# Performance work log

Hardware: AMD Instinct MI355X
Metric: run time of the kernel (lower is better)

## Reference

```python
import jax, jax.numpy as jnp
import numpy as np

B, H, N, D = 4, 4, 2048, 64

def setup_inputs() -> dict:
    key = jax.random.key(0)
    kq, kk, kv, km = jax.random.split(key, 4)
    q = jax.random.normal(kq, (B, H, N, D), dtype=jnp.float32)
    k = jax.random.normal(kk, (B, H, N, D), dtype=jnp.float32)
    v = jax.random.normal(kv, (B, H, N, D), dtype=jnp.float32)
    mask = jax.random.randint(km, (B, N), 0, 2, dtype=jnp.int32)
    return {"q": q, "k": k, "v": v, "mask": mask}

def reference(q, k, v, mask):
    # scores: [B, H, Nq, Nk]
    scale = jnp.asarray(q.shape[-1] ** 0.5, q.dtype)
    scores = jnp.einsum('bhid,bhjd->bhij', q, k) / scale
    neg = jnp.finfo(scores.dtype).min
    m = mask[:, None, None, :]  # [B,1,1,Nk]
    scores = jnp.where(m == 0, neg, scores)
    attention = jax.nn.softmax(scores, axis=-1)
    output = jnp.einsum('bhij,bhjd->bhid', attention, v)
    return (output, attention)
```

## Files before the change

kernel.cpp:

```cpp
#include <hip/hip_runtime.h>

typedef __attribute__((ext_vector_type(8))) short short8;
typedef __attribute__((ext_vector_type(4))) float f32x4;

#define NHEADS 16
#define N_ 2048
#define D_ 64
#define ROWS 16
#define LDP 2056
#define NT 256
#define MT 512

__device__ __forceinline__ unsigned short f2b(float f) {
    unsigned u = __float_as_uint(f);
    return (unsigned short)((u + 0x7FFFu + ((u >> 16) & 1u)) >> 16);
}
__device__ __forceinline__ float b2f(unsigned short b) {
    return __uint_as_float(((unsigned)b) << 16);
}

__global__ __launch_bounds__(NT)
void cvt_bf16_kernel(const float4* __restrict__ src, ushort4* __restrict__ dst, int n4)
{
    int i = blockIdx.x * NT + threadIdx.x;
    if (i < n4) {
        float4 v = src[i];
        ushort4 o;
        o.x = f2b(v.x); o.y = f2b(v.y); o.z = f2b(v.z); o.w = f2b(v.w);
        dst[i] = o;
    }
}

__global__ __launch_bounds__(NT)
void vtrans_kernel(const float* __restrict__ v, unsigned short* __restrict__ vt)
{
    __shared__ float tile[64][65];
    const int head = blockIdx.x >> 5;
    const int k0   = (blockIdx.x & 31) * 64;
    const int tid  = threadIdx.x;

    {
        const int i = tid >> 2;
        const int c = tid & 3;
        const float4* v4 = (const float4*)(v + ((size_t)(head * N_ + k0 + i)) * D_);
        #pragma unroll
        for (int u = 0; u < 4; ++u) {
            const int c4 = c + 4 * u;
            float4 val = v4[c4];
            tile[i][c4 * 4 + 0] = val.x;
            tile[i][c4 * 4 + 1] = val.y;
            tile[i][c4 * 4 + 2] = val.z;
            tile[i][c4 * 4 + 3] = val.w;
        }
    }
    __syncthreads();
    {
        const int d  = tid >> 2;
        const int kk = (tid & 3) * 16;
        unsigned short* dst = vt + ((size_t)(head * D_ + d)) * N_ + k0 + kk;
        #pragma unroll
        for (int m4 = 0; m4 < 4; ++m4) {
            ushort4 ov;
            ov.x = f2b(tile[kk + m4 * 4 + 0][d]);
            ov.y = f2b(tile[kk + m4 * 4 + 1][d]);
            ov.z = f2b(tile[kk + m4 * 4 + 2][d]);
            ov.w = f2b(tile[kk + m4 * 4 + 3][d]);
            *(ushort4*)(dst + m4 * 4) = ov;
        }
    }
}

__global__ __launch_bounds__(MT, 4)
void lg_attn(const unsigned short* __restrict__ Qb,
             const unsigned short* __restrict__ Kb,
             const unsigned short* __restrict__ Vt,
             const int* __restrict__ mask,
             float* __restrict__ out,
             float* __restrict__ attn)
{
    __shared__ unsigned short P[ROWS * LDP];
    __shared__ float wred[128];

    const int tid  = threadIdx.x;
    const int w    = tid >> 6;
    const int lane = tid & 63;
    const int quad = lane >> 4;
    const int l16  = lane & 15;

    const int head = blockIdx.x >> 7;
    const int it   = blockIdx.x & 127;
    const int i0   = it * ROWS;
    const int bidx = head >> 2;

    const unsigned short* qrow = Qb + ((size_t)(head * N_ + i0 + l16)) * D_ + quad * 8;
    const short8 a0 = *(const short8*)qrow;
    const short8 a1 = *(const short8*)(qrow + 32);

    const unsigned short* kbase = Kb + (size_t)head * N_ * D_;
    const int* mrow = mask + bidx * N_;

    float s4[4] = {0.f, 0.f, 0.f, 0.f};
    #pragma unroll 4
    for (int t = 0; t < 16; ++t) {
        const int j0 = (w + 8 * t) * 16;
        const unsigned short* krow = kbase + (size_t)(j0 + l16) * D_ + quad * 8;
        short8 b0 = *(const short8*)krow;
        short8 b1 = *(const short8*)(krow + 32);
        f32x4 cc = {0.f, 0.f, 0.f, 0.f};
        cc = __builtin_amdgcn_mfma_f32_16x16x32_bf16(a0, b0, cc, 0, 0, 0);
        cc = __builtin_amdgcn_mfma_f32_16x16x32_bf16(a1, b1, cc, 0, 0, 0);
        const int mv = mrow[j0 + l16];
        #pragma unroll
        for (int r = 0; r < 4; ++r) {
            const float e = __expf(cc[r] * 0.125f);
            const float p = (mv == 0) ? 0.f : e;
            s4[r] += p;
            P[(quad * 4 + r) * LDP + j0 + l16] = f2b(p);
        }
    }

    #pragma unroll
    for (int r = 0; r < 4; ++r)
        #pragma unroll
        for (int off = 1; off < 16; off <<= 1)
            s4[r] += __shfl_xor(s4[r], off, 64);
    if (l16 == 0) {
        #pragma unroll
        for (int r = 0; r < 4; ++r) wred[w * 16 + quad * 4 + r] = s4[r];
    }
    __syncthreads();

    if (w >= 4) {
        const int tid2 = tid - 256;
        const size_t abase = (size_t)(head * N_ + i0) * N_;
        #pragma unroll 1
        for (int r = 0; r < ROWS; ++r) {
            float s = 0.f;
            #pragma unroll
            for (int ww = 0; ww < 8; ++ww) s += wred[ww * 16 + r];
            const float inv = 1.0f / s;
            f32x4* arow = (f32x4*)(attn + abase + (size_t)r * N_);
            #pragma unroll
            for (int u = 0; u < 2; ++u) {
                const int c4 = tid2 + u * 256;
                ushort4 tv = *(ushort4*)&P[r * LDP + c4 * 4];
                f32x4 f;
                f.x = b2f(tv.x) * inv;
                f.y = b2f(tv.y) * inv;
                f.z = b2f(tv.z) * inv;
                f.w = b2f(tv.w) * inv;
                __builtin_nontemporal_store(f, &arow[c4]);
            }
        }
    } else {
        const int n0 = w * 16;
        const unsigned short* vbase =
            Vt + ((size_t)(head * D_ + n0 + l16)) * N_ + quad * 8;
        f32x4 o = {0.f, 0.f, 0.f, 0.f};
        #pragma unroll 4
        for (int kc = 0; kc < 64; ++kc) {
            short8 ap = *(short8*)&P[l16 * LDP + kc * 32 + quad * 8];
            short8 bv = *(const short8*)(vbase + kc * 32);
            o = __builtin_amdgcn_mfma_f32_16x16x32_bf16(ap, bv, o, 0, 0, 0);
        }
        #pragma unroll
        for (int r = 0; r < 4; ++r) {
            const int row = quad * 4 + r;
            float s = 0.f;
            #pragma unroll
            for (int ww = 0; ww < 8; ++ww) s += wred[ww * 16 + row];
            out[((size_t)(head * N_ + i0 + row)) * D_ + n0 + l16] = o[r] / s;
        }
    }
}

extern "C" void kernel_launch(void* const* d_in, const int* in_sizes, int n_in,
                              void* d_out, int out_size, void* d_ws, size_t ws_size,
                              hipStream_t stream) {
    const float* q    = (const float*)d_in[0];
    const float* k    = (const float*)d_in[1];
    const float* v    = (const float*)d_in[2];
    const int*   mask = (const int*)d_in[3];

    float* out  = (float*)d_out;
    float* attn = out + (size_t)NHEADS * N_ * D_;

    const size_t elems = (size_t)NHEADS * N_ * D_;
    unsigned short* Qb = (unsigned short*)d_ws;
    unsigned short* Kb = Qb + elems;
    unsigned short* Vt = Kb + elems;

    const int n4 = (int)(elems / 4);
    const int cblocks = (n4 + NT - 1) / NT;
    cvt_bf16_kernel<<<cblocks, NT, 0, stream>>>((const float4*)q, (ushort4*)Qb, n4);
    cvt_bf16_kernel<<<cblocks, NT, 0, stream>>>((const float4*)k, (ushort4*)Kb, n4);
    vtrans_kernel<<<NHEADS * 32, NT, 0, stream>>>(v, Vt);

    lg_attn<<<NHEADS * 128, MT, 0, stream>>>(Qb, Kb, Vt, mask, out, attn);
}
```

Measured before the change: 382.4 us.

## Fuse Q conversion into attention kernel and merge K/V prep into one launch

The separate Q fp32-to-bf16 kernel is removed; each attention block now loads Q in fp32 and converts it to bf16 in registers. The K conversion and the V transpose are merged into one prep kernel, which cuts the launch count from four to two. The attention-write loop now reads eight bf16 values per thread with a single 16-byte LDS load and issues two stores. The cost is a slightly larger Q read per block (fp32 instead of bf16), and the prep kernel's K blocks still reserve the shared tile.

```diff
diff --git a/kernel.cpp b/kernel.cpp
--- a/kernel.cpp
+++ b/kernel.cpp
@@ -11,6 +11,9 @@
 #define NT 256
 #define MT 512
 
+#define KCVT_BLOCKS 2048
+#define VT_BLOCKS   512
+
 __device__ __forceinline__ unsigned short f2b(float f) {
     unsigned u = __float_as_uint(f);
     return (unsigned short)((u + 0x7FFFu + ((u >> 16) & 1u)) >> 16);
@@ -20,23 +23,21 @@
 }
 
 __global__ __launch_bounds__(NT)
-void cvt_bf16_kernel(const float4* __restrict__ src, ushort4* __restrict__ dst, int n4)
-{
-    int i = blockIdx.x * NT + threadIdx.x;
-    if (i < n4) {
-        float4 v = src[i];
-        ushort4 o;
-        o.x = f2b(v.x); o.y = f2b(v.y); o.z = f2b(v.z); o.w = f2b(v.w);
-        dst[i] = o;
-    }
-}
-
-__global__ __launch_bounds__(NT)
-void vtrans_kernel(const float* __restrict__ v, unsigned short* __restrict__ vt)
+void prep_kernel(const float4* __restrict__ k, const float* __restrict__ v,
+                 ushort4* __restrict__ Kb, unsigned short* __restrict__ vt)
 {
     __shared__ float tile[64][65];
-    const int head = blockIdx.x >> 5;
-    const int k0   = (blockIdx.x & 31) * 64;
+    if (blockIdx.x < KCVT_BLOCKS) {
+        int i = blockIdx.x * NT + threadIdx.x;
+        float4 val = k[i];
+        ushort4 o;
+        o.x = f2b(val.x); o.y = f2b(val.y); o.z = f2b(val.z); o.w = f2b(val.w);
+        Kb[i] = o;
+        return;
+    }
+    const int b    = blockIdx.x - KCVT_BLOCKS;
+    const int head = b >> 5;
+    const int k0   = (b & 31) * 64;
     const int tid  = threadIdx.x;
 
     {
@@ -71,7 +72,7 @@
 }
 
 __global__ __launch_bounds__(MT, 4)
-void lg_attn(const unsigned short* __restrict__ Qb,
+void lg_attn(const float* __restrict__ Qf,
              const unsigned short* __restrict__ Kb,
              const unsigned short* __restrict__ Vt,
              const int* __restrict__ mask,
@@ -92,9 +93,22 @@
     const int i0   = it * ROWS;
     const int bidx = head >> 2;
 
-    const unsigned short* qrow = Qb + ((size_t)(head * N_ + i0 + l16)) * D_ + quad * 8;
-    const short8 a0 = *(const short8*)qrow;
-    const short8 a1 = *(const short8*)(qrow + 32);
+    short8 a0, a1;
+    {
+        const float* qrow = Qf + ((size_t)(head * N_ + i0 + l16)) * D_ + quad * 8;
+        const float4 q0 = ((const float4*)qrow)[0];
+        const float4 q1 = ((const float4*)qrow)[1];
+        const float4 q2 = ((const float4*)(qrow + 32))[0];
+        const float4 q3 = ((const float4*)(qrow + 32))[1];
+        a0[0] = (short)f2b(q0.x); a0[1] = (short)f2b(q0.y);
+        a0[2] = (short)f2b(q0.z); a0[3] = (short)f2b(q0.w);
+        a0[4] = (short)f2b(q1.x); a0[5] = (short)f2b(q1.y);
+        a0[6] = (short)f2b(q1.z); a0[7] = (short)f2b(q1.w);
+        a1[0] = (short)f2b(q2.x); a1[1] = (short)f2b(q2.y);
+        a1[2] = (short)f2b(q2.z); a1[3] = (short)f2b(q2.w);
+        a1[4] = (short)f2b(q3.x); a1[5] = (short)f2b(q3.y);
+        a1[6] = (short)f2b(q3.z); a1[7] = (short)f2b(q3.w);
+    }
 
     const unsigned short* kbase = Kb + (size_t)head * N_ * D_;
     const int* mrow = mask + bidx * N_;
@@ -140,17 +154,18 @@
             for (int ww = 0; ww < 8; ++ww) s += wred[ww * 16 + r];
             const float inv = 1.0f / s;
             f32x4* arow = (f32x4*)(attn + abase + (size_t)r * N_);
-            #pragma unroll
-            for (int u = 0; u < 2; ++u) {
-                const int c4 = tid2 + u * 256;
-                ushort4 tv = *(ushort4*)&P[r * LDP + c4 * 4];
-                f32x4 f;
-                f.x = b2f(tv.x) * inv;
-                f.y = b2f(tv.y) * inv;
-                f.z = b2f(tv.z) * inv;
-                f.w = b2f(tv.w) * inv;
-                __builtin_nontemporal_store(f, &arow[c4]);
-            }
+            short8 tv = *(short8*)&P[r * LDP + tid2 * 8];
+            f32x4 f0, f1;
+            f0.x = b2f((unsigned short)tv[0]) * inv;
+            f0.y = b2f((unsigned short)tv[1]) * inv;
+            f0.z = b2f((unsigned short)tv[2]) * inv;
+            f0.w = b2f((unsigned short)tv[3]) * inv;
+            f1.x = b2f((unsigned short)tv[4]) * inv;
+            f1.y = b2f((unsigned short)tv[5]) * inv;
+            f1.z = b2f((unsigned short)tv[6]) * inv;
+            f1.w = b2f((unsigned short)tv[7]) * inv;
+            __builtin_nontemporal_store(f0, &arow[tid2 * 2 + 0]);
+            __builtin_nontemporal_store(f1, &arow[tid2 * 2 + 1]);
         }
     } else {
         const int n0 = w * 16;
@@ -186,15 +201,11 @@
     float* attn = out + (size_t)NHEADS * N_ * D_;
 
     const size_t elems = (size_t)NHEADS * N_ * D_;
-    unsigned short* Qb = (unsigned short*)d_ws;
-    unsigned short* Kb = Qb + elems;
+    unsigned short* Kb = (unsigned short*)d_ws;
     unsigned short* Vt = Kb + elems;
 
-    const int n4 = (int)(elems / 4);
-    const int cblocks = (n4 + NT - 1) / NT;
-    cvt_bf16_kernel<<<cblocks, NT, 0, stream>>>((const float4*)q, (ushort4*)Qb, n4);
-    cvt_bf16_kernel<<<cblocks, NT, 0, stream>>>((const float4*)k, (ushort4*)Kb, n4);
-    vtrans_kernel<<<NHEADS * 32, NT, 0, stream>>>(v, Vt);
-
-    lg_attn<<<NHEADS * 128, MT, 0, stream>>>(Qb, Kb, Vt, mask, out, attn);
-}
+    prep_kernel<<<KCVT_BLOCKS + VT_BLOCKS, NT, 0, stream>>>(
+        (const float4*)k, v, (ushort4*)Kb, Vt);
+
+    lg_attn<<<NHEADS * 128, MT, 0, stream>>>(q, Kb, Vt, mask, out, attn);
+}
```

New measurement: 399.5 us. 1.04x slower.
